# Kernel tuning notes

Measured on AMD Instinct MI355X. Metric: run time of the kernel, lower is better.

## Reference

```python
import jax, jax.numpy as jnp
import numpy as np

B, S, D = 4, 2048, 4096
E, R, OUT = 4, 64, 4096
NUM_MOD, NUM_REG, HID = 4, 3, 128
ALPHA = 128.0
SCALING = ALPHA / R  # alpha / rank = 2.0
BALANCE_COEFF = 0.01


def setup_inputs() -> dict:
    key = jax.random.key(0)
    ks = jax.random.split(key, 8)
    return {
        "x": jax.random.normal(ks[0], (B, S, D), jnp.float32),
        "reliability_vec": jax.random.uniform(ks[1], (B, NUM_MOD), jnp.float32),
        "regime_vec": jax.random.uniform(ks[2], (B, NUM_REG), jnp.float32),
        # LoRA experts stacked: A ~ N(0, 1/rank), B random (torch inits B=0; randomized here for a non-trivial baseline)
        "lora_A": jax.random.normal(ks[3], (E, R, D), jnp.float32) / np.sqrt(R).astype(np.float32),
        "lora_B": jax.random.normal(ks[4], (E, OUT, R), jnp.float32) * 0.02,
        # router: Linear(4103->128) -> GELU -> Linear(128->4)
        "w1": jax.random.normal(ks[5], (D + NUM_MOD + NUM_REG, HID), jnp.float32) * 0.02,
        "b1": jnp.zeros((HID,), jnp.float32),
        "w2": jax.random.normal(ks[6], (HID, E), jnp.float32) * 0.02,
        "b2": jnp.zeros((E,), jnp.float32),
    }


def reference(x, reliability_vec, regime_vec, lora_A, lora_B, w1, b1, w2, b2):
    # Router on pooled features + degradation context
    x_pooled = x.mean(axis=1)                                   # [B, D]
    router_in = jnp.concatenate([x_pooled, reliability_vec, regime_vec], axis=-1)
    h = jax.nn.gelu(router_in @ w1 + b1)                        # [B, HID]
    gate_logits = h @ w2 + b2                                   # [B, E]
    gate_probs = jax.nn.softmax(gate_logits, axis=-1)
    top_expert = jnp.argmax(gate_probs, axis=-1)                # [B] int

    # Sparse top-1 dispatch (eval path): gather each sample's expert weights
    A_sel = lora_A[top_expert]                                  # [B, R, D]
    B_sel = lora_B[top_expert]                                  # [B, OUT, R]
    xr = jnp.einsum('bsd,brd->bsr', x, A_sel)                   # [B, S, R]
    out = jnp.einsum('bsr,bor->bso', xr, B_sel) * SCALING       # [B, S, OUT]

    avg_gate = gate_probs.mean(axis=0)
    balance_loss = BALANCE_COEFF * (E * jnp.sum(avg_gate ** 2))
    return out, balance_loss
```

## Files before the change

### kernel.cpp

```cpp
#include <hip/hip_runtime.h>

constexpr int B_ = 4, S_ = 2048, D_ = 4096, E_ = 4, R_ = 64, OUT_ = 4096;
constexpr int NMOD = 4, NREG = 3, HID_ = 128;
constexpr int RIN_ = D_ + NMOD + NREG;
constexpr float SCALING_ = 2.0f;
constexpr int P_   = 128;
constexpr int KC_  = 33;

constexpr size_t WS_PP    = 0;
constexpr size_t WS_HACC2 = WS_PP + (size_t)P_ * B_ * D_;
constexpr size_t WS_TOP   = WS_HACC2 + B_ * KC_ * HID_;
constexpr size_t WS_APK   = WS_TOP + 16;
constexpr size_t WS_BPK   = WS_APK + (size_t)E_ * R_ * D_ / 2;

using short8 = __attribute__((ext_vector_type(8))) short;
using f32x4  = __attribute__((ext_vector_type(4))) float;
union frag_u { int4 i4; short8 s8; };

__device__ inline unsigned short f2bf(float f) {
    unsigned u = __float_as_uint(f);
    unsigned r = u + 0x7FFFu + ((u >> 16) & 1u);
    return (unsigned short)(r >> 16);
}

__global__ __launch_bounds__(256) void prep_kernel(const float* __restrict__ x,
                                                   const float* __restrict__ A,
                                                   const float* __restrict__ Bw,
                                                   float* __restrict__ pp,
                                                   ushort* __restrict__ Apk,
                                                   ushort* __restrict__ Bpk) {
    int bx = blockIdx.x, t = threadIdx.x;
    if (bx < 512) {
        int strip = bx >> 2, b = bx & 3;
        const float4* xp = (const float4*)(x + ((size_t)b * S_ + strip * 16) * D_);
        float4 a0 = {0,0,0,0}, a1 = {0,0,0,0}, a2 = {0,0,0,0}, a3 = {0,0,0,0};
#pragma unroll 4
        for (int r = 0; r < 16; ++r) {
            float4 v0 = xp[(size_t)r * 1024 + t];
            float4 v1 = xp[(size_t)r * 1024 + 256 + t];
            float4 v2 = xp[(size_t)r * 1024 + 512 + t];
            float4 v3 = xp[(size_t)r * 1024 + 768 + t];
            a0.x += v0.x; a0.y += v0.y; a0.z += v0.z; a0.w += v0.w;
            a1.x += v1.x; a1.y += v1.y; a1.z += v1.z; a1.w += v1.w;
            a2.x += v2.x; a2.y += v2.y; a2.z += v2.z; a2.w += v2.w;
            a3.x += v3.x; a3.y += v3.y; a3.z += v3.z; a3.w += v3.w;
        }
        float* ppb = pp + ((size_t)strip * B_ + b) * D_;
        *(float4*)&ppb[(t)       * 4] = a0;
        *(float4*)&ppb[(256 + t) * 4] = a1;
        *(float4*)&ppb[(512 + t) * 4] = a2;
        *(float4*)&ppb[(768 + t) * 4] = a3;
    } else if (bx < 1024) {
        int idx = (bx - 512) * 256 + t;
        int l = idx & 63, n = (idx >> 6) & 3, ks = (idx >> 8) & 127, e = idx >> 15;
        const float* src = A + ((size_t)e * R_ + n * 16 + (l & 15)) * D_
                             + ks * 32 + (l >> 4) * 8;
        float4 v0 = *(const float4*)(src);
        float4 v1 = *(const float4*)(src + 4);
        ushort* dst = Apk + (size_t)idx * 8;
        *(ushort4*)(dst)     = make_ushort4(f2bf(v0.x), f2bf(v0.y), f2bf(v0.z), f2bf(v0.w));
        *(ushort4*)(dst + 4) = make_ushort4(f2bf(v1.x), f2bf(v1.y), f2bf(v1.z), f2bf(v1.w));
    } else {
        int idx = (bx - 1024) * 256 + t;
        int l = idx & 63, kk = (idx >> 6) & 1, nt = (idx >> 7) & 255, e = idx >> 15;
        const float* src = Bw + ((size_t)e * OUT_ + nt * 16 + (l & 15)) * R_
                              + kk * 32 + (l >> 4) * 8;
        float4 v0 = *(const float4*)(src);
        float4 v1 = *(const float4*)(src + 4);
        ushort* dst = Bpk + (size_t)idx * 8;
        *(ushort4*)(dst)     = make_ushort4(f2bf(v0.x), f2bf(v0.y), f2bf(v0.z), f2bf(v0.w));
        *(ushort4*)(dst + 4) = make_ushort4(f2bf(v1.x), f2bf(v1.y), f2bf(v1.z), f2bf(v1.w));
    }
}

__global__ __launch_bounds__(256) void router_h_kernel(const float* __restrict__ pp,
                                                       const float* __restrict__ rel,
                                                       const float* __restrict__ reg,
                                                       const float* __restrict__ w1,
                                                       float* __restrict__ hacc2) {
    __shared__ float rin[128];
    __shared__ float red[256];
    int b = blockIdx.x, kc = blockIdx.y;
    int t = threadIdx.x;
    int k0 = kc * 128;
    {
        int k = k0 + (t & 127), half = t >> 7;
        float s = 0.f;
        if (k < D_) {
            for (int pi = half * 64; pi < half * 64 + 64; ++pi)
                s += pp[((size_t)pi * B_ + b) * D_ + k];
        }
        red[t] = s;
    }
    __syncthreads();
    if (t < 128) {
        int k = k0 + t;
        float v = 0.f;
        if (k < D_)               v = (red[t] + red[t + 128]) * (1.0f / S_);
        else if (k < D_ + NMOD)   v = rel[b * NMOD + (k - D_)];
        else if (k < RIN_)        v = reg[b * NREG + (k - D_ - NMOD)];
        rin[t] = v;
    }
    __syncthreads();
    int h = t & 127, half = t >> 7;
    float acc = 0.f;
#pragma unroll 8
    for (int i = 0; i < 64; ++i) {
        int kk = 2 * i + half;
        int k = k0 + kk;
        if (k < RIN_) acc += rin[kk] * w1[(size_t)k * HID_ + h];
    }
    red[t] = acc;
    __syncthreads();
    if (t < 128)
        hacc2[((size_t)b * KC_ + kc) * HID_ + t] = red[t] + red[t + 128];
}

__global__ void router_finish_kernel(const float* __restrict__ hacc2, const float* __restrict__ b1,
                                     const float* __restrict__ w2, const float* __restrict__ b2,
                                     int* __restrict__ top, float* __restrict__ bal_out) {
    __shared__ float h_lds[B_][HID_];
    __shared__ float logit[B_][E_];
    __shared__ float probs[B_][E_];
    int t = threadIdx.x;
    for (int b = 0; b < B_; ++b) {
        float v = b1[t];
        for (int j = 0; j < KC_; ++j) v += hacc2[((size_t)b * KC_ + j) * HID_ + t];
        float u = 0.7978845608028654f * (v + 0.044715f * v * v * v);
        h_lds[b][t] = 0.5f * v * (1.0f + tanhf(u));
    }
    __syncthreads();
    if (t < B_ * E_) {
        int b = t >> 2, e = t & 3;
        float acc = b2[e];
        for (int j = 0; j < HID_; ++j) acc += h_lds[b][j] * w2[j * E_ + e];
        logit[b][e] = acc;
    }
    __syncthreads();
    if (t < B_) {
        int b = t;
        float mx = logit[b][0]; int arg = 0;
        for (int e = 1; e < E_; ++e) if (logit[b][e] > mx) { mx = logit[b][e]; arg = e; }
        float s = 0.f, pv[E_];
        for (int e = 0; e < E_; ++e) { pv[e] = expf(logit[b][e] - mx); s += pv[e]; }
        for (int e = 0; e < E_; ++e) probs[b][e] = pv[e] / s;
        top[b] = arg;
    }
    __syncthreads();
    if (t == 0) {
        float bal = 0.f;
        for (int e = 0; e < E_; ++e) {
            float avg = 0.25f * (probs[0][e] + probs[1][e] + probs[2][e] + probs[3][e]);
            bal += avg * avg;
        }
        *bal_out = 0.01f * E_ * bal;
    }
}

__global__ __launch_bounds__(512) void xrout_kernel(const float* __restrict__ x,
                                                    const ushort* __restrict__ Apk,
                                                    const ushort* __restrict__ Bpk,
                                                    const int* __restrict__ top,
                                                    float* __restrict__ out) {
    __shared__ ushort xsw[8][16][70];
    __shared__ float  red[8][16][68];
    __shared__ ushort xs2[16][70];
    int sb = blockIdx.x, b = blockIdx.y;
    int e  = top[b];
    int s0 = sb * 16;
    int t = threadIdx.x, l = t & 63, w = t >> 6;
    int kb = w * 512;

    const float* xb = x + ((size_t)b * S_ + s0) * D_;
    const int4*  ap = (const int4*)Apk + (size_t)e * 128 * 4 * 64 + l;
    f32x4 acc[4] = {};
    int lr = l >> 4, lc = l & 15;
    for (int i = 0; i < 8; ++i) {
        int k0 = kb + i * 64;
        float4 xv[4];
#pragma unroll
        for (int j = 0; j < 4; ++j)
            xv[j] = *(const float4*)(xb + (size_t)(lr + 4 * j) * D_ + k0 + lc * 4);
#pragma unroll
        for (int j = 0; j < 4; ++j)
            *(ushort4*)&xsw[w][lr + 4 * j][lc * 4] =
                make_ushort4(f2bf(xv[j].x), f2bf(xv[j].y), f2bf(xv[j].z), f2bf(xv[j].w));
#pragma unroll
        for (int kk = 0; kk < 2; ++kk) {
            short8 xf = *(const short8*)&xsw[w][l & 15][kk * 32 + (l >> 4) * 8];
            int ksg = w * 16 + i * 2 + kk;
#pragma unroll
            for (int n = 0; n < 4; ++n) {
                frag_u af; af.i4 = ap[((size_t)ksg * 4 + n) * 64];
                acc[n] = __builtin_amdgcn_mfma_f32_16x16x32_bf16(xf, af.s8, acc[n], 0, 0, 0);
            }
        }
    }
#pragma unroll
    for (int n = 0; n < 4; ++n)
#pragma unroll
        for (int i = 0; i < 4; ++i)
            red[w][(l >> 4) * 4 + i][n * 16 + (l & 15)] = acc[n][i];
    __syncthreads();
    {
        int row = t >> 5, c2 = (t & 31) * 2;
        float s0f = red[0][row][c2], s1f = red[0][row][c2 + 1];
#pragma unroll
        for (int ks = 1; ks < 8; ++ks) {
            s0f += red[ks][row][c2];
            s1f += red[ks][row][c2 + 1];
        }
        xs2[row][c2]     = f2bf(s0f);
        xs2[row][c2 + 1] = f2bf(s1f);
    }
    __syncthreads();

    short8 xf2[2];
#pragma unroll
    for (int kk = 0; kk < 2; ++kk)
        xf2[kk] = *(const short8*)&xs2[l & 15][kk * 32 + (l >> 4) * 8];
    const int4* bp = (const int4*)Bpk + (size_t)e * 256 * 2 * 64 + l;
    float* ob = out + ((size_t)b * S_ + s0) * OUT_ + w * 512;
    int ro = (l >> 4) * 4, co = l & 15;
#pragma unroll 4
    for (int ntl = 0; ntl < 32; ++ntl) {
        int nt = w * 32 + ntl;
        frag_u bf0, bf1;
        bf0.i4 = bp[((size_t)nt * 2 + 0) * 64];
        bf1.i4 = bp[((size_t)nt * 2 + 1) * 64];
        f32x4 a2 = {};
        a2 = __builtin_amdgcn_mfma_f32_16x16x32_bf16(xf2[0], bf0.s8, a2, 0, 0, 0);
        a2 = __builtin_amdgcn_mfma_f32_16x16x32_bf16(xf2[1], bf1.s8, a2, 0, 0, 0);
#pragma unroll
        for (int i = 0; i < 4; ++i)
            ob[(size_t)(ro + i) * OUT_ + ntl * 16 + co] = a2[i] * SCALING_;
    }
}

extern "C" void kernel_launch(void* const* d_in, const int* in_sizes, int n_in,
                              void* d_out, int out_size, void* d_ws, size_t ws_size,
                              hipStream_t stream) {
    const float* x   = (const float*)d_in[0];
    const float* rel = (const float*)d_in[1];
    const float* reg = (const float*)d_in[2];
    const float* lA  = (const float*)d_in[3];
    const float* lB  = (const float*)d_in[4];
    const float* w1  = (const float*)d_in[5];
    const float* b1  = (const float*)d_in[6];
    const float* w2  = (const float*)d_in[7];
    const float* b2  = (const float*)d_in[8];
    float* out = (float*)d_out;
    float* ws  = (float*)d_ws;

    float*  pp    = ws + WS_PP;
    float*  hacc2 = ws + WS_HACC2;
    int*    top   = (int*)(ws + WS_TOP);
    ushort* Apk   = (ushort*)(ws + WS_APK);
    ushort* Bpk   = (ushort*)(ws + WS_BPK);

    prep_kernel<<<1536, 256, 0, stream>>>(x, lA, lB, pp, Apk, Bpk);
    router_h_kernel<<<dim3(B_, KC_), 256, 0, stream>>>(pp, rel, reg, w1, hacc2);
    router_finish_kernel<<<1, 128, 0, stream>>>(hacc2, b1, w2, b2, top,
                                                out + (size_t)out_size - 1);
    xrout_kernel<<<dim3(S_ / 16, B_), 512, 0, stream>>>(x, Apk, Bpk, top, out);
}
```

Baseline: 108.4 us.

## Fuse router finish into router_h via last-block counter; nontemporal output stores

Removes the separate single-block router_finish launch by having the last router_h block, found through an atomic counter reset in prep_kernel, compute GELU, logits, softmax, top expert and balance loss. The output stores in xrout_kernel switch to nontemporal stores to cut cache pollution on the large fp32 write stream. This saves one launch gap but adds an atomic, fences and a serialized tail inside router_h.

New measurement: 116.2 us. 7.1% more time.

```diff
diff --git a/kernel.cpp b/kernel.cpp
--- a/kernel.cpp
+++ b/kernel.cpp
@@ -10,7 +10,8 @@
 constexpr size_t WS_PP    = 0;
 constexpr size_t WS_HACC2 = WS_PP + (size_t)P_ * B_ * D_;
 constexpr size_t WS_TOP   = WS_HACC2 + B_ * KC_ * HID_;
-constexpr size_t WS_APK   = WS_TOP + 16;
+constexpr size_t WS_CTR   = WS_TOP + 8;
+constexpr size_t WS_APK   = WS_CTR + 8;
 constexpr size_t WS_BPK   = WS_APK + (size_t)E_ * R_ * D_ / 2;
 
 using short8 = __attribute__((ext_vector_type(8))) short;
@@ -28,8 +29,10 @@
                                                    const float* __restrict__ Bw,
                                                    float* __restrict__ pp,
                                                    ushort* __restrict__ Apk,
-                                                   ushort* __restrict__ Bpk) {
+                                                   ushort* __restrict__ Bpk,
+                                                   int* __restrict__ ctr) {
     int bx = blockIdx.x, t = threadIdx.x;
+    if (bx == 0 && t == 0) *ctr = 0;
     if (bx < 512) {
         int strip = bx >> 2, b = bx & 3;
         const float4* xp = (const float4*)(x + ((size_t)b * S_ + strip * 16) * D_);
@@ -77,7 +80,13 @@
                                                        const float* __restrict__ rel,
                                                        const float* __restrict__ reg,
                                                        const float* __restrict__ w1,
-                                                       float* __restrict__ hacc2) {
+                                                       const float* __restrict__ b1,
+                                                       const float* __restrict__ w2,
+                                                       const float* __restrict__ b2,
+                                                       float* __restrict__ hacc2,
+                                                       int* __restrict__ top,
+                                                       float* __restrict__ bal_out,
+                                                       int* __restrict__ ctr) {
     __shared__ float rin[128];
     __shared__ float red[256];
     int b = blockIdx.x, kc = blockIdx.y;
@@ -114,37 +123,41 @@
     __syncthreads();
     if (t < 128)
         hacc2[((size_t)b * KC_ + kc) * HID_ + t] = red[t] + red[t + 128];
-}
-
-__global__ void router_finish_kernel(const float* __restrict__ hacc2, const float* __restrict__ b1,
-                                     const float* __restrict__ w2, const float* __restrict__ b2,
-                                     int* __restrict__ top, float* __restrict__ bal_out) {
+
+    __threadfence();
+    __shared__ int lastf;
+    if (t == 0) lastf = (atomicAdd(ctr, 1) == B_ * KC_ - 1) ? 1 : 0;
+    __syncthreads();
+    if (!lastf) return;
+    __threadfence();
     __shared__ float h_lds[B_][HID_];
     __shared__ float logit[B_][E_];
     __shared__ float probs[B_][E_];
-    int t = threadIdx.x;
-    for (int b = 0; b < B_; ++b) {
-        float v = b1[t];
-        for (int j = 0; j < KC_; ++j) v += hacc2[((size_t)b * KC_ + j) * HID_ + t];
-        float u = 0.7978845608028654f * (v + 0.044715f * v * v * v);
-        h_lds[b][t] = 0.5f * v * (1.0f + tanhf(u));
+    for (int bb = 0; bb < B_; ++bb) {
+        if (t < HID_) {
+            float v = b1[t];
+#pragma unroll 8
+            for (int j = 0; j < KC_; ++j) v += hacc2[((size_t)bb * KC_ + j) * HID_ + t];
+            float u = 0.7978845608028654f * (v + 0.044715f * v * v * v);
+            h_lds[bb][t] = 0.5f * v * (1.0f + tanhf(u));
+        }
     }
     __syncthreads();
     if (t < B_ * E_) {
-        int b = t >> 2, e = t & 3;
-        float acc = b2[e];
-        for (int j = 0; j < HID_; ++j) acc += h_lds[b][j] * w2[j * E_ + e];
-        logit[b][e] = acc;
+        int bb = t >> 2, e = t & 3;
+        float a = b2[e];
+        for (int j = 0; j < HID_; ++j) a += h_lds[bb][j] * w2[j * E_ + e];
+        logit[bb][e] = a;
     }
     __syncthreads();
     if (t < B_) {
-        int b = t;
-        float mx = logit[b][0]; int arg = 0;
-        for (int e = 1; e < E_; ++e) if (logit[b][e] > mx) { mx = logit[b][e]; arg = e; }
+        int bb = t;
+        float mx = logit[bb][0]; int arg = 0;
+        for (int e = 1; e < E_; ++e) if (logit[bb][e] > mx) { mx = logit[bb][e]; arg = e; }
         float s = 0.f, pv[E_];
-        for (int e = 0; e < E_; ++e) { pv[e] = expf(logit[b][e] - mx); s += pv[e]; }
-        for (int e = 0; e < E_; ++e) probs[b][e] = pv[e] / s;
-        top[b] = arg;
+        for (int e = 0; e < E_; ++e) { pv[e] = expf(logit[bb][e] - mx); s += pv[e]; }
+        for (int e = 0; e < E_; ++e) probs[bb][e] = pv[e] / s;
+        top[bb] = arg;
     }
     __syncthreads();
     if (t == 0) {
@@ -233,7 +246,8 @@
         a2 = __builtin_amdgcn_mfma_f32_16x16x32_bf16(xf2[1], bf1.s8, a2, 0, 0, 0);
 #pragma unroll
         for (int i = 0; i < 4; ++i)
-            ob[(size_t)(ro + i) * OUT_ + ntl * 16 + co] = a2[i] * SCALING_;
+            __builtin_nontemporal_store(a2[i] * SCALING_,
+                                        &ob[(size_t)(ro + i) * OUT_ + ntl * 16 + co]);
     }
 }
 
@@ -255,12 +269,13 @@
     float*  pp    = ws + WS_PP;
     float*  hacc2 = ws + WS_HACC2;
     int*    top   = (int*)(ws + WS_TOP);
+    int*    ctr   = (int*)(ws + WS_CTR);
     ushort* Apk   = (ushort*)(ws + WS_APK);
     ushort* Bpk   = (ushort*)(ws + WS_BPK);
 
-    prep_kernel<<<1536, 256, 0, stream>>>(x, lA, lB, pp, Apk, Bpk);
-    router_h_kernel<<<dim3(B_, KC_), 256, 0, stream>>>(pp, rel, reg, w1, hacc2);
-    router_finish_kernel<<<1, 128, 0, stream>>>(hacc2, b1, w2, b2, top,
-                                                out + (size_t)out_size - 1);
+    prep_kernel<<<1536, 256, 0, stream>>>(x, lA, lB, pp, Apk, Bpk, ctr);
+    router_h_kernel<<<dim3(B_, KC_), 256, 0, stream>>>(pp, rel, reg, w1, b1, w2, b2,
+                                                       hacc2, top,
+                                                       out + (size_t)out_size - 1, ctr);
     xrout_kernel<<<dim3(S_ / 16, B_), 512, 0, stream>>>(x, Apk, Bpk, top, out);
 }
```
